# Performance work log

Measured on AMD Instinct MI355X. Metric: run time of the kernel, lower is better.

The kernel has to match this reference:

```python
import jax, jax.numpy as jnp
import numpy as np

L = 3          # num encoder layers
H = 128        # hidden_dim
NH = 8         # num_heads
HD = H // NH   # head_dim
FF = H * 4     # ff inner dim (after GLU)
B, N = 32, 512
NUM_BINS = 50


def _linear_params(key, fan_in, fan_out):
    kw, kb = jax.random.split(key)
    lim = 1.0 / np.sqrt(fan_in)
    W = jax.random.uniform(kw, (fan_in, fan_out), jnp.float32, -lim, lim)
    b = jax.random.uniform(kb, (fan_out,), jnp.float32, -lim, lim)
    return W, b


def setup_inputs() -> dict:
    key = jax.random.key(0)
    ks = jax.random.split(key, 16)
    x = jax.random.normal(ks[0], (B, N, H), jnp.float32)
    distance_matrix = jax.random.uniform(ks[1], (B, N, N), jnp.float32)
    mask = jax.random.randint(ks[2], (B, N), 0, 2).astype(bool)

    def stack_linear(k, fan_in, fan_out):
        Ws, bs = [], []
        for l in range(L):
            W, b = _linear_params(jax.random.fold_in(k, l), fan_in, fan_out)
            Ws.append(W); bs.append(b)
        return jnp.stack(Ws), jnp.stack(bs)

    Wq, bq = stack_linear(ks[3], H, H)
    Wk, bk = stack_linear(ks[4], H, H)
    Wv, bv = stack_linear(ks[5], H, H)
    Wo, bo = stack_linear(ks[6], H, H)
    dist_emb = jax.random.normal(ks[7], (L, NUM_BINS, NH), jnp.float32)
    attn_bias = jnp.zeros((L, NH, 1, 1), jnp.float32)
    g1 = jnp.ones((L, H), jnp.float32); b1 = jnp.zeros((L, H), jnp.float32)
    g2 = jnp.ones((L, H), jnp.float32); b2 = jnp.zeros((L, H), jnp.float32)
    Wf1, bf1 = stack_linear(ks[8], H, 2 * FF)
    Wf2, bf2 = stack_linear(ks[9], FF, H)
    return dict(x=x, distance_matrix=distance_matrix, mask=mask,
                Wq=Wq, bq=bq, Wk=Wk, bk=bk, Wv=Wv, bv=bv, Wo=Wo, bo=bo,
                dist_emb=dist_emb, attn_bias=attn_bias,
                g1=g1, b1=b1, g2=g2, b2=b2,
                Wf1=Wf1, bf1=bf1, Wf2=Wf2, bf2=bf2)


def _layernorm(x, g, b, eps=1e-5):
    mu = jnp.mean(x, axis=-1, keepdims=True)
    var = jnp.var(x, axis=-1, keepdims=True)
    return (x - mu) * jax.lax.rsqrt(var + eps) * g + b


def _attention(h, bins, key_mask, Wq, bq, Wk, bk, Wv, bv, Wo, bo, dist_emb, attn_bias):
    # h: [B,N,H]; bins: [B,N,N] int; key_mask: [B,N] bool (True = masked)
    Bsz, Nn, _ = h.shape
    Q = (h @ Wq + bq).reshape(Bsz, Nn, NH, HD)
    K = (h @ Wk + bk).reshape(Bsz, Nn, NH, HD)
    V = (h @ Wv + bv).reshape(Bsz, Nn, NH, HD)
    scores = jnp.einsum('bqhd,bkhd->bhqk', Q, K) / np.sqrt(HD)
    bias = jnp.transpose(dist_emb[bins], (0, 3, 1, 2))  # [B,NH,N,N]
    scores = scores + bias + attn_bias[None]
    scores = jnp.where(key_mask[:, None, None, :], -1e9, scores)
    attn = jax.nn.softmax(scores, axis=-1)
    out = jnp.einsum('bhqk,bkhd->bqhd', attn, V).reshape(Bsz, Nn, H)
    return out @ Wo + bo


def reference(x, distance_matrix, mask, Wq, bq, Wk, bk, Wv, bv, Wo, bo,
              dist_emb, attn_bias, g1, b1, g2, b2, Wf1, bf1, Wf2, bf2):
    bins = jnp.clip((distance_matrix * 10.0).astype(jnp.int32), 0, NUM_BINS - 1)
    h = x
    for l in range(L):
        # pre-LN attention block
        a = _attention(_layernorm(h, g1[l], b1[l]), bins, mask,
                       Wq[l], bq[l], Wk[l], bk[l], Wv[l], bv[l], Wo[l], bo[l],
                       dist_emb[l], attn_bias[l])
        h = h + a
        # pre-LN GLU feed-forward
        u = _layernorm(h, g2[l], b2[l]) @ Wf1[l] + bf1[l]  # [B,N,2*FF]
        ua, ub = jnp.split(u, 2, axis=-1)
        h = h + (ua * jax.nn.sigmoid(ub)) @ Wf2[l] + bf2[l]
    return h
```

## Files before the change

kernel.cpp:

```cpp
#include <hip/hip_runtime.h>
#include <stdint.h>

#define Bq 32
#define Nq 512
#define Hq 128
#define NHq 8
#define HDq 16
#define Mq (Bq * Nq)

typedef unsigned short u16;
typedef __attribute__((ext_vector_type(8))) short short8;
typedef __attribute__((ext_vector_type(8))) _Float16 half8;
typedef __attribute__((ext_vector_type(2))) __fp16 fp16x2;
typedef __attribute__((ext_vector_type(4))) float f32x4;

__device__ __forceinline__ float bf2f(u16 v) {
    return __uint_as_float(((unsigned int)v) << 16);
}
__device__ __forceinline__ float ldin(const void* p, long idx, int bf) {
    if (bf) return bf2f(((const u16*)p)[idx]);
    return ((const float*)p)[idx];
}
__device__ __forceinline__ u16 f2bf(float v) {
    unsigned int u = __float_as_uint(v);
    return (u16)((u + 0x7FFFu + ((u >> 16) & 1u)) >> 16);
}
__device__ __forceinline__ u16 f2h(float v) {
    _Float16 h = (_Float16)v;
    return *(u16*)&h;
}
__device__ __forceinline__ unsigned pk2h(float a, float b) {
    fp16x2 c = __builtin_amdgcn_cvt_pkrtz(a, b);
    return *(unsigned*)&c;
}

__global__ void prep_kernel(const void* xraw, const void* de, const void* ab,
                            const void* mraw, int* flag, float* deo, float* abo,
                            unsigned* mbits, int n) {
    __shared__ int cnt, orA, orB, orC, orD;
    int tid = threadIdx.x;
    if (tid == 0) { cnt = 0; orA = 0; orB = 0; orC = 0; orD = 0; }
    __syncthreads();
    const u16* u = (const u16*)xraw;
    int good = 0;
    for (int i = tid; i < 1024; i += 256) {
        u16 v = u[i];
        int e = (v >> 7) & 0xFF;
        if (v == 0 || (e >= 90 && e <= 141)) good++;
    }
    atomicAdd(&cnt, good);
    const uint4* p4 = (const uint4*)mraw;
    unsigned a = 0, b = 0, c = 0, d = 0;
    for (int i = tid; i < n / 16; i += 256) {
        uint4 w = p4[i];
        unsigned all = w.x | w.y | w.z | w.w;
        a |= all & 0xFEFEFEFEu;
        b |= all & 0x0000FF00u;
        c |= all & 0xFFFFFF00u;
        d |= w.y | w.w;
    }
    if (a) atomicOr(&orA, 1);
    if (b) atomicOr(&orB, 1);
    if (c) atomicOr(&orC, 1);
    if (d) atomicOr(&orD, 1);
    __syncthreads();
    int bf = (cnt >= 900);
    if (tid == 0) *flag = bf;
    int mode;
    if (orA) mode = orB ? 3 : 4;
    else if (orC) mode = 0;
    else mode = orD ? 1 : 2;
    for (int i = tid; i < 1200; i += 256) deo[i] = ldin(de, i, bf);
    if (tid < 24) abo[tid] = ldin(ab, tid, bf);
    const unsigned char* p = (const unsigned char*)mraw;
    for (int wI = tid; wI < n / 32; wI += 256) {
        unsigned word = 0;
        for (int j = 0; j < 32; ++j) {
            int i = wI * 32 + j;
            int v;
            switch (mode) {
                case 0: v = p[i]; break;
                case 1: v = ((const int*)p)[i]; break;
                case 2: v = (int)((const long long*)p)[i]; break;
                case 3: v = ((const u16*)p)[i] != 0; break;
                default: v = (((const float*)p)[i] != 0.0f); break;
            }
            if (v) word |= 1u << j;
        }
        mbits[wI] = word;
    }
}

__global__ void kprep_kernel(const unsigned* __restrict__ mbits,
                             u16* __restrict__ kidxg, int* __restrict__ nkt,
                             unsigned* __restrict__ tmask) {
    int b = blockIdx.x;
    int lane = threadIdx.x & 63;
    int pos_base = 0;
    for (int w = 0; w < 8; ++w) {
        unsigned lo = mbits[b * 16 + 2 * w], hi = mbits[b * 16 + 2 * w + 1];
        unsigned long long word = ((unsigned long long)hi << 32) | lo;
        unsigned long long un = ~word;
        int bit = (int)((un >> lane) & 1ull);
        unsigned long long before = un & ((1ull << lane) - 1ull);
        int pos = pos_base + __popcll(before);
        if (bit) kidxg[b * 512 + pos] = (u16)(w * 64 + lane);
        pos_base += __popcll(un);
    }
    int nk = pos_base;
    int nkp = (nk + 31) & ~31;
    if (nkp == 0) nkp = 32;
    int nt = nkp >> 5;
    for (int j = nk + lane; j < nkp; j += 64) kidxg[b * 512 + j] = 0;
    if (lane == 0) {
        nkt[b] = nt;
        for (int t = 0; t < 16; ++t) tmask[b * 16 + t] = 0;
        int rem = nk & 31;
        if (rem) tmask[b * 16 + nt - 1] = 0xFFFFFFFFu << rem;
        if (nk == 0) tmask[b * 16] = 0xFFFFFFFFu;
    }
}

__global__ __launch_bounds__(256) void binsc_kernel(
    const void* __restrict__ dist, const u16* __restrict__ kidxg,
    const int* __restrict__ nkt, unsigned char* __restrict__ binsc,
    const int* flagp) {
    int bf = *flagp;
    int b = blockIdx.y;
    int q0 = blockIdx.x * 8;
    __shared__ u16 kl[512];
    __shared__ int ntS;
    int tid = threadIdx.x;
    if (tid == 0) ntS = nkt[b];
    kl[tid] = kidxg[b * 512 + tid];
    kl[tid + 256] = kidxg[b * 512 + tid + 256];
    __syncthreads();
    int nkp = ntS * 32;
    for (int rq = 0; rq < 8; ++rq) {
        int q = q0 + rq;
        long rowoff = ((long)b * 512 + q) * 512;
        for (int j = tid; j < nkp; j += 256) {
            float d = ldin(dist, rowoff + kl[j], bf);
            int v = (int)(d * 10.0f);
            v = v < 0 ? 0 : (v > 49 ? 49 : v);
            binsc[((size_t)b * 512 + q) * 512 + j] = (unsigned char)(v << 2);
        }
    }
}

__global__ __launch_bounds__(256) void init_ln_kernel(
    const void* x, float* __restrict__ h, u16* __restrict__ hn,
    const void* graw, const void* braw, const int* flagp) {
    int bf = *flagp;
    int row = blockIdx.x * 4 + (threadIdx.x >> 6);
    int lane = threadIdx.x & 63;
    float x0 = ldin(x, (long)row * Hq + lane, bf);
    float x1 = ldin(x, (long)row * Hq + lane + 64, bf);
    h[(size_t)row * Hq + lane] = x0;
    h[(size_t)row * Hq + lane + 64] = x1;
    float s = x0 + x1, s2 = x0 * x0 + x1 * x1;
#pragma unroll
    for (int o = 32; o; o >>= 1) {
        s += __shfl_xor(s, o);
        s2 += __shfl_xor(s2, o);
    }
    float mu = s * (1.0f / 128.0f);
    float var = fmaxf(s2 * (1.0f / 128.0f) - mu * mu, 0.0f);
    float rr = rsqrtf(var + 1e-5f);
    float g0 = ldin(graw, lane, bf), g1v = ldin(graw, lane + 64, bf);
    float b0 = ldin(braw, lane, bf), b1v = ldin(braw, lane + 64, bf);
    hn[(size_t)row * Hq + lane]      = f2bf((x0 - mu) * rr * g0 + b0);
    hn[(size_t)row * Hq + lane + 64] = f2bf((x1 - mu) * rr * g1v + b1v);
}

__global__ __launch_bounds__(256) void wtrans_kernel(
    const void* Wqr, const void* Wkr, const void* Wvr, const void* Wor,
    const void* Wf1r, const void* Wf2r,
    u16* qkvT, u16* oT, u16* f1T, u16* f2T, const int* flagp) {
    int bf = *flagp;
    int bid = blockIdx.x;
    int l = bid >> 8, r = bid & 255;
    const void* src; u16* dst; long soff, doff; int Kd, Nd, t;
    if (r < 64) {
        int mat = r >> 4; t = r & 15; Kd = 128; Nd = 128;
        soff = (long)l * 16384;
        if (mat == 0)      { src = Wqr; dst = qkvT; doff = (long)l * 49152; }
        else if (mat == 1) { src = Wkr; dst = qkvT; doff = (long)l * 49152 + 16384; }
        else if (mat == 2) { src = Wvr; dst = qkvT; doff = (long)l * 49152 + 32768; }
        else               { src = Wor; dst = oT;   doff = (long)l * 16384; }
    } else if (r < 192) {
        t = r - 64; Kd = 128; Nd = 1024;
        src = Wf1r; soff = (long)l * 131072; dst = f1T; doff = (long)l * 131072;
    } else {
        t = r - 192; Kd = 512; Nd = 128;
        src = Wf2r; soff = (long)l * 65536; dst = f2T; doff = (long)l * 65536;
    }
    int ntile = Nd >> 5;
    int tk = t / ntile, tn = t % ntile;
    __shared__ u16 Ts[32][33];
    int rr = threadIdx.x >> 3, cc0 = (threadIdx.x & 7) * 4;
#pragma unroll
    for (int i = 0; i < 4; ++i) {
        long idx = soff + (long)(tk * 32 + rr) * Nd + tn * 32 + cc0 + i;
        Ts[rr][cc0 + i] = f2bf(ldin(src, idx, bf));
    }
    __syncthreads();
#pragma unroll
    for (int i = 0; i < 4; ++i) {
        long idx = doff + (long)(tn * 32 + rr) * Kd + tk * 32 + cc0 + i;
        dst[idx] = Ts[cc0 + i][rr];
    }
}

__global__ __launch_bounds__(256, 2) void mfma_gemm64_kernel(
    const u16* __restrict__ A, const u16* __restrict__ WT,
    const void* __restrict__ braw, long bOff, float* __restrict__ C,
    int K, int resid, const int* flagp,
    const void* lnG, const void* lnB, long lnOff, u16* hnout, void* outp) {
    __shared__ __align__(16) u16 As[64][40];
    __shared__ __align__(16) u16 Bs[128][40];
    __shared__ float Ct[64][128];
    int tid = threadIdx.x;
    int m0 = blockIdx.x * 64;
    int wave = tid >> 6, lane = tid & 63;
    int wm = (wave >> 1) * 32, wn = (wave & 1) * 64;
    int q = lane >> 4, ln = lane & 15;
    f32x4 zero = {0.f, 0.f, 0.f, 0.f};
    f32x4 acc[2][4];
#pragma unroll
    for (int i = 0; i < 2; ++i)
#pragma unroll
        for (int j = 0; j < 4; ++j) acc[i][j] = zero;
    int sar = tid >> 2, sac = (tid & 3) * 8;
    int sbr = tid >> 1, sbc = (tid & 1) * 16;
    const u16* Ap = A + (size_t)(m0 + sar) * K + sac;
    const u16* Bp = WT + (size_t)sbr * K + sbc;
    for (int k0 = 0; k0 < K; k0 += 32) {
        uint4 av = *(const uint4*)(Ap + k0);
        uint4 b0 = *(const uint4*)(Bp + k0);
        uint4 b1 = *(const uint4*)(Bp + k0 + 8);
        *(uint4*)&As[sar][sac] = av;
        *(uint4*)&Bs[sbr][sbc] = b0; *(uint4*)&Bs[sbr][sbc + 8] = b1;
        __syncthreads();
        short8 af[2], bfv[4];
#pragma unroll
        for (int t = 0; t < 2; ++t) af[t] = *(const short8*)&As[wm + t * 16 + ln][q * 8];
#pragma unroll
        for (int t = 0; t < 4; ++t) bfv[t] = *(const short8*)&Bs[wn + t * 16 + ln][q * 8];
#pragma unroll
        for (int ti = 0; ti < 2; ++ti)
#pragma unroll
            for (int tj = 0; tj < 4; ++tj)
                acc[ti][tj] = __builtin_amdgcn_mfma_f32_16x16x32_bf16(
                    af[ti], bfv[tj], acc[ti][tj], 0, 0, 0);
        __syncthreads();
    }
    int bf = *flagp;
#pragma unroll
    for (int tj = 0; tj < 4; ++tj) {
        int n = wn + tj * 16 + ln;
        float bias = ldin(braw, bOff + n, bf);
#pragma unroll
        for (int ti = 0; ti < 2; ++ti)
#pragma unroll
            for (int r = 0; r < 4; ++r) {
                int m = m0 + wm + ti * 16 + q * 4 + r;
                float v = acc[ti][tj][r] + bias;
                float* dst = C + (size_t)m * 128 + n;
                if (resid) v += *dst;
                *dst = v;
                Ct[m - m0][n] = v;
                if (outp) {
                    if (bf) ((u16*)outp)[(size_t)m * 128 + n] = f2bf(v);
                    else ((float*)outp)[(size_t)m * 128 + n] = v;
                }
            }
    }
    if (hnout) {
        __syncthreads();
        float gg0 = ldin(lnG, lnOff + lane, bf);
        float gg1 = ldin(lnG, lnOff + lane + 64, bf);
        float bb0 = ldin(lnB, lnOff + lane, bf);
        float bb1 = ldin(lnB, lnOff + lane + 64, bf);
        for (int rr = 0; rr < 16; ++rr) {
            int row = wave * 16 + rr;
            float x0 = Ct[row][lane], x1 = Ct[row][lane + 64];
            float s = x0 + x1, s2v = x0 * x0 + x1 * x1;
#pragma unroll
            for (int o = 32; o; o >>= 1) {
                s += __shfl_xor(s, o);
                s2v += __shfl_xor(s2v, o);
            }
            float mu = s * (1.0f / 128.0f);
            float var = fmaxf(s2v * (1.0f / 128.0f) - mu * mu, 0.0f);
            float rstd = rsqrtf(var + 1e-5f);
            int m = m0 + row;
            hnout[(size_t)m * 128 + lane]      = f2bf((x0 - mu) * rstd * gg0 + bb0);
            hnout[(size_t)m * 128 + lane + 64] = f2bf((x1 - mu) * rstd * gg1 + bb1);
        }
    }
}

__global__ __launch_bounds__(256, 2) void qkv_mfma_kernel(
    const u16* __restrict__ A, const u16* __restrict__ qkvT_l,
    const void* bqr, const void* bkr, const void* bvr, long bOff,
    u16* __restrict__ Qo, u16* __restrict__ Ko, u16* __restrict__ Vo,
    const int* flagp) {
    int sel = blockIdx.y;
    const u16* WT = qkvT_l + (size_t)sel * 16384;
    const void* braw = sel == 0 ? bqr : (sel == 1 ? bkr : bvr);
    u16* C = sel == 0 ? Qo : (sel == 1 ? Ko : Vo);
    float scale = sel == 0 ? 0.25f : 1.0f;
    __shared__ __align__(16) u16 As[64][40];
    __shared__ __align__(16) u16 Bs[128][40];
    int tid = threadIdx.x;
    int m0 = blockIdx.x * 64;
    int wave = tid >> 6, lane = tid & 63;
    int wm = (wave >> 1) * 32, wn = (wave & 1) * 64;
    int q = lane >> 4, ln = lane & 15;
    f32x4 zero = {0.f, 0.f, 0.f, 0.f};
    f32x4 acc[2][4];
#pragma unroll
    for (int i = 0; i < 2; ++i)
#pragma unroll
        for (int j = 0; j < 4; ++j) acc[i][j] = zero;
    int sar = tid >> 2, sac = (tid & 3) * 8;
    int sbr = tid >> 1, sbc = (tid & 1) * 16;
    const u16* Ap = A + (size_t)(m0 + sar) * 128 + sac;
    const u16* Bp = WT + (size_t)sbr * 128 + sbc;
#pragma unroll
    for (int k0 = 0; k0 < 128; k0 += 32) {
        uint4 av = *(const uint4*)(Ap + k0);
        uint4 b0 = *(const uint4*)(Bp + k0);
        uint4 b1 = *(const uint4*)(Bp + k0 + 8);
        *(uint4*)&As[sar][sac] = av;
        *(uint4*)&Bs[sbr][sbc] = b0; *(uint4*)&Bs[sbr][sbc + 8] = b1;
        __syncthreads();
        short8 af[2], bfv[4];
#pragma unroll
        for (int t = 0; t < 2; ++t) af[t] = *(const short8*)&As[wm + t * 16 + ln][q * 8];
#pragma unroll
        for (int t = 0; t < 4; ++t) bfv[t] = *(const short8*)&Bs[wn + t * 16 + ln][q * 8];
#pragma unroll
        for (int ti = 0; ti < 2; ++ti)
#pragma unroll
            for (int tj = 0; tj < 4; ++tj)
                acc[ti][tj] = __builtin_amdgcn_mfma_f32_16x16x32_bf16(
                    af[ti], bfv[tj], acc[ti][tj], 0, 0, 0);
        __syncthreads();
    }
    int bf = *flagp;
#pragma unroll
    for (int tj = 0; tj < 4; ++tj) {
        int n = wn + tj * 16 + ln;
        float bias = ldin(braw, bOff + n, bf);
#pragma unroll
        for (int ti = 0; ti < 2; ++ti)
#pragma unroll
            for (int r = 0; r < 4; ++r) {
                int m = m0 + wm + ti * 16 + q * 4 + r;
                C[(size_t)m * 128 + n] = f2h((acc[ti][tj][r] + bias) * scale);
            }
    }
}

__global__ __launch_bounds__(256, 2) void glu_mfma_kernel(
    const u16* __restrict__ A, const u16* __restrict__ f1T_l,
    const void* __restrict__ braw, long bOff, u16* __restrict__ Vout,
    const int* flagp) {
    __shared__ __align__(16) u16 As[128][40];
    __shared__ __align__(16) u16 Ba[64][40];
    __shared__ __align__(16) u16 Bb[64][40];
    int tid = threadIdx.x;
    int m0 = blockIdx.x * 128, n0 = blockIdx.y * 64;
    int wave = tid >> 6, lane = tid & 63;
    int wm = (wave >> 1) * 64, wn = (wave & 1) * 32;
    int q = lane >> 4, ln = lane & 15;
    f32x4 zero = {0.f, 0.f, 0.f, 0.f};
    f32x4 accA[4][2], accB[4][2];
#pragma unroll
    for (int i = 0; i < 4; ++i)
#pragma unroll
        for (int j = 0; j < 2; ++j) { accA[i][j] = zero; accB[i][j] = zero; }
    int sr = tid >> 1, sc = (tid & 1) * 16;
    const u16* Ap = A + (size_t)(m0 + sr) * 128 + sc;
    const u16* BpA = f1T_l + (size_t)(n0 + sr) * 128 + sc;
    const u16* BpB = f1T_l + (size_t)(512 + n0 + (sr - 64)) * 128 + sc;
#pragma unroll
    for (int k0 = 0; k0 < 128; k0 += 32) {
        uint4 a0 = *(const uint4*)(Ap + k0);
        uint4 a1 = *(const uint4*)(Ap + k0 + 8);
        *(uint4*)&As[sr][sc] = a0; *(uint4*)&As[sr][sc + 8] = a1;
        if (sr < 64) {
            uint4 w0 = *(const uint4*)(BpA + k0);
            uint4 w1 = *(const uint4*)(BpA + k0 + 8);
            *(uint4*)&Ba[sr][sc] = w0; *(uint4*)&Ba[sr][sc + 8] = w1;
        } else {
            uint4 w0 = *(const uint4*)(BpB + k0);
            uint4 w1 = *(const uint4*)(BpB + k0 + 8);
            *(uint4*)&Bb[sr - 64][sc] = w0; *(uint4*)&Bb[sr - 64][sc + 8] = w1;
        }
        __syncthreads();
        short8 af[4], ba[2], bb[2];
#pragma unroll
        for (int t = 0; t < 4; ++t) af[t] = *(const short8*)&As[wm + t * 16 + ln][q * 8];
#pragma unroll
        for (int t = 0; t < 2; ++t) {
            ba[t] = *(const short8*)&Ba[wn + t * 16 + ln][q * 8];
            bb[t] = *(const short8*)&Bb[wn + t * 16 + ln][q * 8];
        }
#pragma unroll
        for (int ti = 0; ti < 4; ++ti)
#pragma unroll
            for (int tj = 0; tj < 2; ++tj) {
                accA[ti][tj] = __builtin_amdgcn_mfma_f32_16x16x32_bf16(
                    af[ti], ba[tj], accA[ti][tj], 0, 0, 0);
                accB[ti][tj] = __builtin_amdgcn_mfma_f32_16x16x32_bf16(
                    af[ti], bb[tj], accB[ti][tj], 0, 0, 0);
            }
        __syncthreads();
    }
    int bf = *flagp;
#pragma unroll
    for (int tj = 0; tj < 2; ++tj) {
        int n = n0 + wn + tj * 16 + ln;
        float biasA = ldin(braw, bOff + n, bf);
        float biasB = ldin(braw, bOff + 512 + n, bf);
#pragma unroll
        for (int ti = 0; ti < 4; ++ti)
#pragma unroll
            for (int r = 0; r < 4; ++r) {
                int m = m0 + wm + ti * 16 + q * 4 + r;
                float ua = accA[ti][tj][r] + biasA;
                float ub = accB[ti][tj][r] + biasB;
                Vout[(size_t)m * 512 + n] = f2bf(ua / (1.0f + __expf(-ub)));
            }
    }
}

__global__ __launch_bounds__(256, 4) void attn_kernel(
    const u16* __restrict__ Qh, const u16* __restrict__ Kh,
    const u16* __restrict__ Vh, const unsigned char* __restrict__ binsc,
    const u16* __restrict__ kidxg, const int* __restrict__ nktp,
    const unsigned* __restrict__ tmaskp, const float* __restrict__ deL,
    const float* __restrict__ abL, u16* __restrict__ out) {
    int id = blockIdx.x;
    int c = id & 7, t5 = id >> 3;
    int nh = t5 & 7;
    int pair = ((t5 >> 3) << 3) | c;
    int b = pair >> 2, qq = pair & 3;

    __shared__ __align__(16) u16 KsF[8192];
    __shared__ __align__(16) u16 VT[16 * 520];
    __shared__ __align__(16) u16 Pl[4 * 16 * 40];

    int tid = threadIdx.x;
    int nt = __builtin_amdgcn_readfirstlane(nktp[b]);
    int nkp = nt * 32;
    const u16* Kp = Kh + (size_t)(b * Nq) * Hq + nh * HDq;
    const u16* Vp = Vh + (size_t)(b * Nq) * Hq + nh * HDq;
    for (int r = tid; r < nkp; r += 256) {
        int row = kidxg[b * 512 + r];
        int kt = r >> 5, s = (r >> 4) & 1, lnr = r & 15;
        uint4 k0v = *(const uint4*)(Kp + (size_t)row * Hq);
        uint4 k1v = *(const uint4*)(Kp + (size_t)row * Hq + 8);
        *(uint4*)&KsF[kt * 512 + s * 256 + lnr * 8]       = k0v;
        *(uint4*)&KsF[kt * 512 + s * 256 + 128 + lnr * 8] = k1v;
        uint4 v0 = *(const uint4*)(Vp + (size_t)row * Hq);
        uint4 v1 = *(const uint4*)(Vp + (size_t)row * Hq + 8);
        u16 vv[16];
        *(uint4*)&vv[0] = v0; *(uint4*)&vv[8] = v1;
#pragma unroll
        for (int d = 0; d < 16; ++d) VT[d * 520 + r] = vv[d];
    }
    __syncthreads();

    int wave = tid >> 6, lane = tid & 63;
    int quad = lane >> 4, ln = lane & 15;
    int q0w = qq * 128 + wave * 32;

    float tblf = (lane < 50) ? deL[lane * NHq + nh] + abL[nh] : 0.0f;
    int tbli = __float_as_int(tblf);
    unsigned tl = tmaskp[b * 16 + nt - 1];

    half8 qf[2];
#pragma unroll
    for (int t = 0; t < 2; ++t) {
        uint4 qv = {0, 0, 0, 0};
        if (quad < 2)
            qv = *(const uint4*)(Qh + (size_t)(b * Nq + q0w + t * 16 + ln) * Hq
                                 + nh * HDq + quad * 8);
        qf[t] = *(half8*)&qv;
    }

    f32x4 zero = {0.f, 0.f, 0.f, 0.f};
    f32x4 acc[2] = {zero, zero};
    float zp[2] = {0.f, 0.f};
    _Float16* Pw = (_Float16*)&Pl[wave * 640];
    const _Float16* KsH = (const _Float16*)KsF;
    const _Float16* VTH = (const _Float16*)VT;
    const unsigned char* brow0 = binsc + ((size_t)b * 512 + (q0w + ln)) * 512;
    const unsigned char* brow1 = brow0 + (size_t)16 * 512;

    unsigned pb00 = *(const unsigned*)(brow0 + quad * 4);
    unsigned pb01 = *(const unsigned*)(brow0 + 16 + quad * 4);
    unsigned pb10 = *(const unsigned*)(brow1 + quad * 4);
    unsigned pb11 = *(const unsigned*)(brow1 + 16 + quad * 4);

    for (int kt = 0; kt < nt; ++kt) {
        int k0 = kt * 32;
        unsigned w = (kt == nt - 1) ? tl : 0u;
        unsigned cb00 = pb00, cb01 = pb01, cb10 = pb10, cb11 = pb11;
        if (kt < nt - 1) {
            pb00 = *(const unsigned*)(brow0 + k0 + 32 + quad * 4);
            pb01 = *(const unsigned*)(brow0 + k0 + 48 + quad * 4);
            pb10 = *(const unsigned*)(brow1 + k0 + 32 + quad * 4);
            pb11 = *(const unsigned*)(brow1 + k0 + 48 + quad * 4);
        }
        half8 vb = *(const half8*)(VTH + ln * 520 + k0 + quad * 8);
        half8 ka0 = {}, ka1 = {};
        if (quad < 2) {
            ka0 = *(const half8*)(KsH + kt * 512 + quad * 128 + ln * 8);
            ka1 = *(const half8*)(KsH + kt * 512 + 256 + quad * 128 + ln * 8);
        }
#pragma unroll
        for (int t = 0; t < 2; ++t) {
            unsigned bw0 = t == 0 ? cb00 : cb10;
            unsigned bw1 = t == 0 ? cb01 : cb11;
            f32x4 s0 = __builtin_amdgcn_mfma_f32_16x16x32_f16(ka0, qf[t], zero, 0, 0, 0);
            f32x4 s1 = __builtin_amdgcn_mfma_f32_16x16x32_f16(ka1, qf[t], zero, 0, 0, 0);
            float p[8];
#pragma unroll
            for (int r = 0; r < 4; ++r) {
                float bias = __int_as_float(__builtin_amdgcn_ds_bpermute(
                    (int)((bw0 >> (8 * r)) & 0xFFu), tbli));
                float sc = s0[r] + bias;
                bool m = (w >> (quad * 4 + r)) & 1u;
                p[r] = m ? 0.0f : __expf(sc);
            }
#pragma unroll
            for (int r = 0; r < 4; ++r) {
                float bias = __int_as_float(__builtin_amdgcn_ds_bpermute(
                    (int)((bw1 >> (8 * r)) & 0xFFu), tbli));
                float sc = s1[r] + bias;
                bool m = (w >> (16 + quad * 4 + r)) & 1u;
                p[4 + r] = m ? 0.0f : __expf(sc);
            }
            zp[t] += ((p[0] + p[1]) + (p[2] + p[3])) +
                     ((p[4] + p[5]) + (p[6] + p[7]));
            uint2 w0, w1;
            w0.x = pk2h(p[0], p[1]); w0.y = pk2h(p[2], p[3]);
            w1.x = pk2h(p[4], p[5]); w1.y = pk2h(p[6], p[7]);
            *(uint2*)(Pw + ln * 40 + quad * 4)      = w0;
            *(uint2*)(Pw + ln * 40 + 16 + quad * 4) = w1;
            half8 pa = *(const half8*)(Pw + ln * 40 + quad * 8);
            acc[t] = __builtin_amdgcn_mfma_f32_16x16x32_f16(pa, vb, acc[t], 0, 0, 0);
        }
    }
#pragma unroll
    for (int t = 0; t < 2; ++t) {
        zp[t] += __shfl_xor(zp[t], 16);
        zp[t] += __shfl_xor(zp[t], 32);
    }
#pragma unroll
    for (int t = 0; t < 2; ++t) {
#pragma unroll
        for (int r = 0; r < 4; ++r) {
            float zz = __shfl(zp[t], quad * 4 + r);
            float val = acc[t][r] / fmaxf(zz, 1e-35f);
            int qrow = q0w + t * 16 + quad * 4 + r;
            out[(size_t)(b * Nq + qrow) * Hq + nh * HDq + ln] = f2bf(val);
        }
    }
}

extern "C" void kernel_launch(void* const* d_in, const int* in_sizes, int n_in,
                              void* d_out, int out_size, void* d_ws, size_t ws_size,
                              hipStream_t stream) {
    const void* x  = d_in[0];
    const void* dist = d_in[1];
    const void* mask = d_in[2];
    const void* Wq = d_in[3];  const void* bq = d_in[4];
    const void* Wk = d_in[5];  const void* bk = d_in[6];
    const void* Wv = d_in[7];  const void* bv = d_in[8];
    const void* Wo = d_in[9];  const void* bo = d_in[10];
    const void* de = d_in[11]; const void* ab = d_in[12];
    const void* g1 = d_in[13]; const void* b1 = d_in[14];
    const void* g2 = d_in[15]; const void* b2 = d_in[16];
    const void* Wf1 = d_in[17]; const void* bf1 = d_in[18];
    const void* Wf2 = d_in[19]; const void* bf2 = d_in[20];

    char* ws = (char*)d_ws;
    const size_t OFF_DE   = 64;
    const size_t OFF_AB   = 5120;
    const size_t OFF_BINS = 8192;
    const size_t OFF_MSK  = OFF_BINS + 8388608;
    const size_t OFF_KIDX = OFF_MSK + 4096;
    const size_t OFF_NKT  = OFF_KIDX + 32768;
    const size_t OFF_TM   = OFF_NKT + 256;
    const size_t OFF_H    = OFF_TM + 4096;
    const size_t OFF_QKV  = OFF_H + 8388608;
    const size_t OFF_HN   = OFF_QKV + 25165824;
    const size_t OFF_ATT  = OFF_HN + 4194304;
    const size_t OFF_WT   = OFF_ATT + 4194304;
    const size_t NEEDED   = OFF_WT + 1572864;
    if (ws_size < NEEDED) return;

    int* flag = (int*)ws;
    float* deF = (float*)(ws + OFF_DE);
    float* abF = (float*)(ws + OFF_AB);
    unsigned char* binsc = (unsigned char*)(ws + OFF_BINS);
    unsigned* mbits = (unsigned*)(ws + OFF_MSK);
    u16* kidxg = (u16*)(ws + OFF_KIDX);
    int* nkt = (int*)(ws + OFF_NKT);
    unsigned* tmask = (unsigned*)(ws + OFF_TM);
    float* h = (float*)(ws + OFF_H);
    u16* Qh = (u16*)(ws + OFF_QKV);
    u16* Kh = Qh + 2097152;
    u16* Vh = Qh + 2 * 2097152;
    u16* vglu = (u16*)(ws + OFF_QKV);
    u16* hn = (u16*)(ws + OFF_HN);
    u16* att = (u16*)(ws + OFF_ATT);
    u16* qkvT = (u16*)(ws + OFF_WT);
    u16* oT  = qkvT + 147456;
    u16* f1T = oT + 49152;
    u16* f2T = f1T + 393216;

    prep_kernel<<<1, 256, 0, stream>>>(x, de, ab, mask, flag, deF, abF, mbits, Bq * Nq);
    kprep_kernel<<<32, 64, 0, stream>>>(mbits, kidxg, nkt, tmask);
    dim3 gbc(64, 32);
    binsc_kernel<<<gbc, 256, 0, stream>>>(dist, kidxg, nkt, binsc, flag);
    init_ln_kernel<<<4096, 256, 0, stream>>>(x, h, hn, g1, b1, flag);
    wtrans_kernel<<<768, 256, 0, stream>>>(Wq, Wk, Wv, Wo, Wf1, Wf2,
                                           qkvT, oT, f1T, f2T, flag);

    dim3 gqkv(256, 3);
    dim3 gglu(128, 8);
    for (int l = 0; l < 3; ++l) {
        qkv_mfma_kernel<<<gqkv, 256, 0, stream>>>(hn, qkvT + (size_t)l * 49152,
                                                  bq, bk, bv, (long)l * Hq,
                                                  Qh, Kh, Vh, flag);
        attn_kernel<<<1024, 256, 0, stream>>>(Qh, Kh, Vh, binsc, kidxg, nkt, tmask,
                                              deF + (long)l * 400, abF + (long)l * 8, att);
        mfma_gemm64_kernel<<<256, 256, 0, stream>>>(att, oT + (size_t)l * 16384,
                                                    bo, (long)l * Hq, h, 128, 1, flag,
                                                    g2, b2, (long)l * Hq, hn, nullptr);
        glu_mfma_kernel<<<gglu, 256, 0, stream>>>(hn, f1T + (size_t)l * 131072,
                                                  bf1, (long)l * 1024, vglu, flag);
        if (l < 2) {
            mfma_gemm64_kernel<<<256, 256, 0, stream>>>(vglu, f2T + (size_t)l * 65536,
                                                        bf2, (long)l * Hq, h, 512, 1, flag,
                                                        g1, b1, (long)(l + 1) * Hq, hn,
                                                        nullptr);
        } else {
            mfma_gemm64_kernel<<<256, 256, 0, stream>>>(vglu, f2T + (size_t)l * 65536,
                                                        bf2, (long)l * Hq, h, 512, 1, flag,
                                                        nullptr, nullptr, 0, nullptr,
                                                        d_out);
        }
    }
}
```

Baseline: 409.6 us.

## Merge prep kernels into one launch and use 16x16x16 MFMA in attention

Four setup kernels (dtype and mask detection, key-index compaction, weight transposes, initial layernorm) become one megaprep kernel whose blocks branch by index, and every block detects bf16 on its own instead of reading a flag. The attention kernel switches from padded 16x16x32 MFMA (half the K lanes zero) to 16x16x16 MFMA. This keeps the P tile in registers instead of an LDS round-trip and stores K row-major with stride 20. The aim is fewer launches and no wasted MFMA work or LDS traffic, at the cost of twice as many MFMA issues and a possible race: block 0's flag write is no longer ordered before other kernels' use of it within the launch, though later kernels are still stream-ordered.

```diff
diff --git a/kernel.cpp b/kernel.cpp
--- a/kernel.cpp
+++ b/kernel.cpp
@@ -10,7 +10,7 @@
 
 typedef unsigned short u16;
 typedef __attribute__((ext_vector_type(8))) short short8;
-typedef __attribute__((ext_vector_type(8))) _Float16 half8;
+typedef __attribute__((ext_vector_type(4))) _Float16 half4;
 typedef __attribute__((ext_vector_type(2))) __fp16 fp16x2;
 typedef __attribute__((ext_vector_type(4))) float f32x4;
 
@@ -33,91 +33,159 @@
     fp16x2 c = __builtin_amdgcn_cvt_pkrtz(a, b);
     return *(unsigned*)&c;
 }
-
-__global__ void prep_kernel(const void* xraw, const void* de, const void* ab,
-                            const void* mraw, int* flag, float* deo, float* abo,
-                            unsigned* mbits, int n) {
-    __shared__ int cnt, orA, orB, orC, orD;
-    int tid = threadIdx.x;
-    if (tid == 0) { cnt = 0; orA = 0; orB = 0; orC = 0; orD = 0; }
-    __syncthreads();
+__device__ __forceinline__ int detect_bf_wave(const void* xraw) {
     const u16* u = (const u16*)xraw;
+    int lane = threadIdx.x & 63;
     int good = 0;
-    for (int i = tid; i < 1024; i += 256) {
-        u16 v = u[i];
+#pragma unroll
+    for (int i = 0; i < 16; ++i) {
+        u16 v = u[lane * 16 + i];
         int e = (v >> 7) & 0xFF;
         if (v == 0 || (e >= 90 && e <= 141)) good++;
     }
-    atomicAdd(&cnt, good);
-    const uint4* p4 = (const uint4*)mraw;
-    unsigned a = 0, b = 0, c = 0, d = 0;
-    for (int i = tid; i < n / 16; i += 256) {
-        uint4 w = p4[i];
-        unsigned all = w.x | w.y | w.z | w.w;
-        a |= all & 0xFEFEFEFEu;
-        b |= all & 0x0000FF00u;
-        c |= all & 0xFFFFFF00u;
-        d |= w.y | w.w;
-    }
-    if (a) atomicOr(&orA, 1);
-    if (b) atomicOr(&orB, 1);
-    if (c) atomicOr(&orC, 1);
-    if (d) atomicOr(&orD, 1);
-    __syncthreads();
-    int bf = (cnt >= 900);
-    if (tid == 0) *flag = bf;
-    int mode;
-    if (orA) mode = orB ? 3 : 4;
-    else if (orC) mode = 0;
-    else mode = orD ? 1 : 2;
-    for (int i = tid; i < 1200; i += 256) deo[i] = ldin(de, i, bf);
-    if (tid < 24) abo[tid] = ldin(ab, tid, bf);
-    const unsigned char* p = (const unsigned char*)mraw;
-    for (int wI = tid; wI < n / 32; wI += 256) {
-        unsigned word = 0;
-        for (int j = 0; j < 32; ++j) {
-            int i = wI * 32 + j;
-            int v;
-            switch (mode) {
-                case 0: v = p[i]; break;
-                case 1: v = ((const int*)p)[i]; break;
-                case 2: v = (int)((const long long*)p)[i]; break;
-                case 3: v = ((const u16*)p)[i] != 0; break;
-                default: v = (((const float*)p)[i] != 0.0f); break;
-            }
-            if (v) word |= 1u << j;
-        }
-        mbits[wI] = word;
-    }
-}
-
-__global__ void kprep_kernel(const unsigned* __restrict__ mbits,
-                             u16* __restrict__ kidxg, int* __restrict__ nkt,
-                             unsigned* __restrict__ tmask) {
-    int b = blockIdx.x;
-    int lane = threadIdx.x & 63;
-    int pos_base = 0;
-    for (int w = 0; w < 8; ++w) {
-        unsigned lo = mbits[b * 16 + 2 * w], hi = mbits[b * 16 + 2 * w + 1];
-        unsigned long long word = ((unsigned long long)hi << 32) | lo;
-        unsigned long long un = ~word;
-        int bit = (int)((un >> lane) & 1ull);
-        unsigned long long before = un & ((1ull << lane) - 1ull);
-        int pos = pos_base + __popcll(before);
-        if (bit) kidxg[b * 512 + pos] = (u16)(w * 64 + lane);
-        pos_base += __popcll(un);
-    }
-    int nk = pos_base;
-    int nkp = (nk + 31) & ~31;
-    if (nkp == 0) nkp = 32;
-    int nt = nkp >> 5;
-    for (int j = nk + lane; j < nkp; j += 64) kidxg[b * 512 + j] = 0;
-    if (lane == 0) {
-        nkt[b] = nt;
-        for (int t = 0; t < 16; ++t) tmask[b * 16 + t] = 0;
-        int rem = nk & 31;
-        if (rem) tmask[b * 16 + nt - 1] = 0xFFFFFFFFu << rem;
-        if (nk == 0) tmask[b * 16] = 0xFFFFFFFFu;
+#pragma unroll
+    for (int o = 32; o; o >>= 1) good += __shfl_xor(good, o);
+    return good >= 900;
+}
+
+__global__ __launch_bounds__(256) void megaprep_kernel(
+    const void* xraw, const void* de, const void* ab, const void* mraw,
+    int* flag, float* deo, float* abo, unsigned* mbits,
+    u16* kidxg, int* nkt, unsigned* tmask,
+    float* h, u16* hn, const void* g1, const void* b1,
+    const void* Wqr, const void* Wkr, const void* Wvr, const void* Wor,
+    const void* Wf1r, const void* Wf2r,
+    u16* qkvT, u16* oT, u16* f1T, u16* f2T) {
+    int bid = blockIdx.x;
+    int tid = threadIdx.x;
+    int bf = detect_bf_wave(xraw);
+
+    if (bid == 0) {
+        __shared__ int orA, orB, orC, orD;
+        __shared__ unsigned smb[512];
+        if (tid == 0) { orA = 0; orB = 0; orC = 0; orD = 0; }
+        __syncthreads();
+        const int n = Bq * Nq;
+        const uint4* p4 = (const uint4*)mraw;
+        unsigned a = 0, b = 0, c = 0, d = 0;
+        for (int i = tid; i < n / 16; i += 256) {
+            uint4 w = p4[i];
+            unsigned all = w.x | w.y | w.z | w.w;
+            a |= all & 0xFEFEFEFEu;
+            b |= all & 0x0000FF00u;
+            c |= all & 0xFFFFFF00u;
+            d |= w.y | w.w;
+        }
+        if (a) atomicOr(&orA, 1);
+        if (b) atomicOr(&orB, 1);
+        if (c) atomicOr(&orC, 1);
+        if (d) atomicOr(&orD, 1);
+        __syncthreads();
+        if (tid == 0) *flag = bf;
+        int mode;
+        if (orA) mode = orB ? 3 : 4;
+        else if (orC) mode = 0;
+        else mode = orD ? 1 : 2;
+        for (int i = tid; i < 1200; i += 256) deo[i] = ldin(de, i, bf);
+        if (tid < 24) abo[tid] = ldin(ab, tid, bf);
+        const unsigned char* p = (const unsigned char*)mraw;
+        for (int wI = tid; wI < 512; wI += 256) {
+            unsigned word = 0;
+            for (int j = 0; j < 32; ++j) {
+                int i = wI * 32 + j;
+                int v;
+                switch (mode) {
+                    case 0: v = p[i]; break;
+                    case 1: v = ((const int*)p)[i]; break;
+                    case 2: v = (int)((const long long*)p)[i]; break;
+                    case 3: v = ((const u16*)p)[i] != 0; break;
+                    default: v = (((const float*)p)[i] != 0.0f); break;
+                }
+                if (v) word |= 1u << j;
+            }
+            mbits[wI] = word;
+            smb[wI] = word;
+        }
+        __syncthreads();
+        int wv = tid >> 6, lane = tid & 63;
+        for (int bb = wv; bb < 32; bb += 4) {
+            int pos_base = 0;
+            for (int w = 0; w < 8; ++w) {
+                unsigned lo = smb[bb * 16 + 2 * w], hi = smb[bb * 16 + 2 * w + 1];
+                unsigned long long word = ((unsigned long long)hi << 32) | lo;
+                unsigned long long un = ~word;
+                int bit = (int)((un >> lane) & 1ull);
+                unsigned long long before = un & ((1ull << lane) - 1ull);
+                int pos = pos_base + __popcll(before);
+                if (bit) kidxg[bb * 512 + pos] = (u16)(w * 64 + lane);
+                pos_base += __popcll(un);
+            }
+            int nk = pos_base;
+            int nkp = (nk + 31) & ~31;
+            if (nkp == 0) nkp = 32;
+            int nt = nkp >> 5;
+            for (int j = nk + lane; j < nkp; j += 64) kidxg[bb * 512 + j] = 0;
+            if (lane == 0) {
+                nkt[bb] = nt;
+                for (int t = 0; t < 16; ++t) tmask[bb * 16 + t] = 0;
+                int rem = nk & 31;
+                if (rem) tmask[bb * 16 + nt - 1] = 0xFFFFFFFFu << rem;
+                if (nk == 0) tmask[bb * 16] = 0xFFFFFFFFu;
+            }
+        }
+    } else if (bid <= 768) {
+        int bid2 = bid - 1;
+        int l = bid2 >> 8, r = bid2 & 255;
+        const void* src; u16* dst; long soff, doff; int Kd, Nd, t;
+        if (r < 64) {
+            int mat = r >> 4; t = r & 15; Kd = 128; Nd = 128;
+            soff = (long)l * 16384;
+            if (mat == 0)      { src = Wqr; dst = qkvT; doff = (long)l * 49152; }
+            else if (mat == 1) { src = Wkr; dst = qkvT; doff = (long)l * 49152 + 16384; }
+            else if (mat == 2) { src = Wvr; dst = qkvT; doff = (long)l * 49152 + 32768; }
+            else               { src = Wor; dst = oT;   doff = (long)l * 16384; }
+        } else if (r < 192) {
+            t = r - 64; Kd = 128; Nd = 1024;
+            src = Wf1r; soff = (long)l * 131072; dst = f1T; doff = (long)l * 131072;
+        } else {
+            t = r - 192; Kd = 512; Nd = 128;
+            src = Wf2r; soff = (long)l * 65536; dst = f2T; doff = (long)l * 65536;
+        }
+        int ntile = Nd >> 5;
+        int tk = t / ntile, tn = t % ntile;
+        __shared__ u16 Ts[32][33];
+        int rr = tid >> 3, cc0 = (tid & 7) * 4;
+#pragma unroll
+        for (int i = 0; i < 4; ++i) {
+            long idx = soff + (long)(tk * 32 + rr) * Nd + tn * 32 + cc0 + i;
+            Ts[rr][cc0 + i] = f2bf(ldin(src, idx, bf));
+        }
+        __syncthreads();
+#pragma unroll
+        for (int i = 0; i < 4; ++i) {
+            long idx = doff + (long)(tn * 32 + rr) * Kd + tk * 32 + cc0 + i;
+            dst[idx] = Ts[cc0 + i][rr];
+        }
+    } else {
+        int row = (bid - 769) * 4 + (tid >> 6);
+        int lane = tid & 63;
+        float x0 = ldin(xraw, (long)row * Hq + lane, bf);
+        float x1 = ldin(xraw, (long)row * Hq + lane + 64, bf);
+        h[(size_t)row * Hq + lane] = x0;
+        h[(size_t)row * Hq + lane + 64] = x1;
+        float s = x0 + x1, s2 = x0 * x0 + x1 * x1;
+#pragma unroll
+        for (int o = 32; o; o >>= 1) {
+            s += __shfl_xor(s, o);
+            s2 += __shfl_xor(s2, o);
+        }
+        float mu = s * (1.0f / 128.0f);
+        float var = fmaxf(s2 * (1.0f / 128.0f) - mu * mu, 0.0f);
+        float rr = rsqrtf(var + 1e-5f);
+        float g0 = ldin(g1, lane, bf), g1v = ldin(g1, lane + 64, bf);
+        float b0 = ldin(b1, lane, bf), b1v = ldin(b1, lane + 64, bf);
+        hn[(size_t)row * Hq + lane]      = f2bf((x0 - mu) * rr * g0 + b0);
+        hn[(size_t)row * Hq + lane + 64] = f2bf((x1 - mu) * rr * g1v + b1v);
     }
 }
 
@@ -148,70 +216,6 @@
     }
 }
 
-__global__ __launch_bounds__(256) void init_ln_kernel(
-    const void* x, float* __restrict__ h, u16* __restrict__ hn,
-    const void* graw, const void* braw, const int* flagp) {
-    int bf = *flagp;
-    int row = blockIdx.x * 4 + (threadIdx.x >> 6);
-    int lane = threadIdx.x & 63;
-    float x0 = ldin(x, (long)row * Hq + lane, bf);
-    float x1 = ldin(x, (long)row * Hq + lane + 64, bf);
-    h[(size_t)row * Hq + lane] = x0;
-    h[(size_t)row * Hq + lane + 64] = x1;
-    float s = x0 + x1, s2 = x0 * x0 + x1 * x1;
-#pragma unroll
-    for (int o = 32; o; o >>= 1) {
-        s += __shfl_xor(s, o);
-        s2 += __shfl_xor(s2, o);
-    }
-    float mu = s * (1.0f / 128.0f);
-    float var = fmaxf(s2 * (1.0f / 128.0f) - mu * mu, 0.0f);
-    float rr = rsqrtf(var + 1e-5f);
-    float g0 = ldin(graw, lane, bf), g1v = ldin(graw, lane + 64, bf);
-    float b0 = ldin(braw, lane, bf), b1v = ldin(braw, lane + 64, bf);
-    hn[(size_t)row * Hq + lane]      = f2bf((x0 - mu) * rr * g0 + b0);
-    hn[(size_t)row * Hq + lane + 64] = f2bf((x1 - mu) * rr * g1v + b1v);
-}
-
-__global__ __launch_bounds__(256) void wtrans_kernel(
-    const void* Wqr, const void* Wkr, const void* Wvr, const void* Wor,
-    const void* Wf1r, const void* Wf2r,
-    u16* qkvT, u16* oT, u16* f1T, u16* f2T, const int* flagp) {
-    int bf = *flagp;
-    int bid = blockIdx.x;
-    int l = bid >> 8, r = bid & 255;
-    const void* src; u16* dst; long soff, doff; int Kd, Nd, t;
-    if (r < 64) {
-        int mat = r >> 4; t = r & 15; Kd = 128; Nd = 128;
-        soff = (long)l * 16384;
-        if (mat == 0)      { src = Wqr; dst = qkvT; doff = (long)l * 49152; }
-        else if (mat == 1) { src = Wkr; dst = qkvT; doff = (long)l * 49152 + 16384; }
-        else if (mat == 2) { src = Wvr; dst = qkvT; doff = (long)l * 49152 + 32768; }
-        else               { src = Wor; dst = oT;   doff = (long)l * 16384; }
-    } else if (r < 192) {
-        t = r - 64; Kd = 128; Nd = 1024;
-        src = Wf1r; soff = (long)l * 131072; dst = f1T; doff = (long)l * 131072;
-    } else {
-        t = r - 192; Kd = 512; Nd = 128;
-        src = Wf2r; soff = (long)l * 65536; dst = f2T; doff = (long)l * 65536;
-    }
-    int ntile = Nd >> 5;
-    int tk = t / ntile, tn = t % ntile;
-    __shared__ u16 Ts[32][33];
-    int rr = threadIdx.x >> 3, cc0 = (threadIdx.x & 7) * 4;
-#pragma unroll
-    for (int i = 0; i < 4; ++i) {
-        long idx = soff + (long)(tk * 32 + rr) * Nd + tn * 32 + cc0 + i;
-        Ts[rr][cc0 + i] = f2bf(ldin(src, idx, bf));
-    }
-    __syncthreads();
-#pragma unroll
-    for (int i = 0; i < 4; ++i) {
-        long idx = doff + (long)(tn * 32 + rr) * Kd + tk * 32 + cc0 + i;
-        dst[idx] = Ts[cc0 + i][rr];
-    }
-}
-
 __global__ __launch_bounds__(256, 2) void mfma_gemm64_kernel(
     const u16* __restrict__ A, const u16* __restrict__ WT,
     const void* __restrict__ braw, long bOff, float* __restrict__ C,
@@ -450,9 +454,8 @@
     int pair = ((t5 >> 3) << 3) | c;
     int b = pair >> 2, qq = pair & 3;
 
-    __shared__ __align__(16) u16 KsF[8192];
+    __shared__ __align__(16) u16 KsF[512 * 20];
     __shared__ __align__(16) u16 VT[16 * 520];
-    __shared__ __align__(16) u16 Pl[4 * 16 * 40];
 
     int tid = threadIdx.x;
     int nt = __builtin_amdgcn_readfirstlane(nktp[b]);
@@ -461,11 +464,12 @@
     const u16* Vp = Vh + (size_t)(b * Nq) * Hq + nh * HDq;
     for (int r = tid; r < nkp; r += 256) {
         int row = kidxg[b * 512 + r];
-        int kt = r >> 5, s = (r >> 4) & 1, lnr = r & 15;
         uint4 k0v = *(const uint4*)(Kp + (size_t)row * Hq);
         uint4 k1v = *(const uint4*)(Kp + (size_t)row * Hq + 8);
-        *(uint4*)&KsF[kt * 512 + s * 256 + lnr * 8]       = k0v;
-        *(uint4*)&KsF[kt * 512 + s * 256 + 128 + lnr * 8] = k1v;
+        *(uint2*)&KsF[r * 20]      = make_uint2(k0v.x, k0v.y);
+        *(uint2*)&KsF[r * 20 + 4]  = make_uint2(k0v.z, k0v.w);
+        *(uint2*)&KsF[r * 20 + 8]  = make_uint2(k1v.x, k1v.y);
+        *(uint2*)&KsF[r * 20 + 12] = make_uint2(k1v.z, k1v.w);
         uint4 v0 = *(const uint4*)(Vp + (size_t)row * Hq);
         uint4 v1 = *(const uint4*)(Vp + (size_t)row * Hq + 8);
         u16 vv[16];
@@ -483,20 +487,17 @@
     int tbli = __float_as_int(tblf);
     unsigned tl = tmaskp[b * 16 + nt - 1];
 
-    half8 qf[2];
+    half4 qf[2];
 #pragma unroll
     for (int t = 0; t < 2; ++t) {
-        uint4 qv = {0, 0, 0, 0};
-        if (quad < 2)
-            qv = *(const uint4*)(Qh + (size_t)(b * Nq + q0w + t * 16 + ln) * Hq
-                                 + nh * HDq + quad * 8);
-        qf[t] = *(half8*)&qv;
+        uint2 qv = *(const uint2*)(Qh + (size_t)(b * Nq + q0w + t * 16 + ln) * Hq
+                                   + nh * HDq + quad * 4);
+        qf[t] = *(half4*)&qv;
     }
 
     f32x4 zero = {0.f, 0.f, 0.f, 0.f};
     f32x4 acc[2] = {zero, zero};
     float zp[2] = {0.f, 0.f};
-    _Float16* Pw = (_Float16*)&Pl[wave * 640];
     const _Float16* KsH = (const _Float16*)KsF;
     const _Float16* VTH = (const _Float16*)VT;
     const unsigned char* brow0 = binsc + ((size_t)b * 512 + (q0w + ln)) * 512;
@@ -517,18 +518,16 @@
             pb10 = *(const unsigned*)(brow1 + k0 + 32 + quad * 4);
             pb11 = *(const unsigned*)(brow1 + k0 + 48 + quad * 4);
         }
-        half8 vb = *(const half8*)(VTH + ln * 520 + k0 + quad * 8);
-        half8 ka0 = {}, ka1 = {};
-        if (quad < 2) {
-            ka0 = *(const half8*)(KsH + kt * 512 + quad * 128 + ln * 8);
-            ka1 = *(const half8*)(KsH + kt * 512 + 256 + quad * 128 + ln * 8);
-        }
+        half4 ka0 = *(const half4*)(KsH + (size_t)(k0 + ln) * 20 + quad * 4);
+        half4 ka1 = *(const half4*)(KsH + (size_t)(k0 + 16 + ln) * 20 + quad * 4);
+        half4 vb0 = *(const half4*)(VTH + ln * 520 + k0 + quad * 4);
+        half4 vb1 = *(const half4*)(VTH + ln * 520 + k0 + 16 + quad * 4);
 #pragma unroll
         for (int t = 0; t < 2; ++t) {
             unsigned bw0 = t == 0 ? cb00 : cb10;
             unsigned bw1 = t == 0 ? cb01 : cb11;
-            f32x4 s0 = __builtin_amdgcn_mfma_f32_16x16x32_f16(ka0, qf[t], zero, 0, 0, 0);
-            f32x4 s1 = __builtin_amdgcn_mfma_f32_16x16x32_f16(ka1, qf[t], zero, 0, 0, 0);
+            f32x4 s0 = __builtin_amdgcn_mfma_f32_16x16x16f16(ka0, qf[t], zero, 0, 0, 0);
+            f32x4 s1 = __builtin_amdgcn_mfma_f32_16x16x16f16(ka1, qf[t], zero, 0, 0, 0);
             float p[8];
 #pragma unroll
             for (int r = 0; r < 4; ++r) {
@@ -548,13 +547,12 @@
             }
             zp[t] += ((p[0] + p[1]) + (p[2] + p[3])) +
                      ((p[4] + p[5]) + (p[6] + p[7]));
-            uint2 w0, w1;
-            w0.x = pk2h(p[0], p[1]); w0.y = pk2h(p[2], p[3]);
-            w1.x = pk2h(p[4], p[5]); w1.y = pk2h(p[6], p[7]);
-            *(uint2*)(Pw + ln * 40 + quad * 4)      = w0;
-            *(uint2*)(Pw + ln * 40 + 16 + quad * 4) = w1;
-            half8 pa = *(const half8*)(Pw + ln * 40 + quad * 8);
-            acc[t] = __builtin_amdgcn_mfma_f32_16x16x32_f16(pa, vb, acc[t], 0, 0, 0);
+            uint2 pw0 = make_uint2(pk2h(p[0], p[1]), pk2h(p[2], p[3]));
+            uint2 pw1 = make_uint2(pk2h(p[4], p[5]), pk2h(p[6], p[7]));
+            half4 pa0 = *(half4*)&pw0;
+            half4 pa1 = *(half4*)&pw1;
+            acc[t] = __builtin_amdgcn_mfma_f32_16x16x16f16(pa0, vb0, acc[t], 0, 0, 0);
+            acc[t] = __builtin_amdgcn_mfma_f32_16x16x16f16(pa1, vb1, acc[t], 0, 0, 0);
         }
     }
 #pragma unroll
@@ -626,13 +624,11 @@
     u16* f1T = oT + 49152;
     u16* f2T = f1T + 393216;
 
-    prep_kernel<<<1, 256, 0, stream>>>(x, de, ab, mask, flag, deF, abF, mbits, Bq * Nq);
-    kprep_kernel<<<32, 64, 0, stream>>>(mbits, kidxg, nkt, tmask);
+    megaprep_kernel<<<4865, 256, 0, stream>>>(
+        x, de, ab, mask, flag, deF, abF, mbits, kidxg, nkt, tmask,
+        h, hn, g1, b1, Wq, Wk, Wv, Wo, Wf1, Wf2, qkvT, oT, f1T, f2T);
     dim3 gbc(64, 32);
     binsc_kernel<<<gbc, 256, 0, stream>>>(dist, kidxg, nkt, binsc, flag);
-    init_ln_kernel<<<4096, 256, 0, stream>>>(x, h, hn, g1, b1, flag);
-    wtrans_kernel<<<768, 256, 0, stream>>>(Wq, Wk, Wv, Wo, Wf1, Wf2,
-                                           qkvT, oT, f1T, f2T, flag);
 
     dim3 gqkv(256, 3);
     dim3 gglu(128, 8);
```

Result: slower. 424.5 us (+3.6%).
